# Optimization experiments

Hardware: AMD Instinct MI355X
Metric: run time of the kernel (lower is better)

The kernel has to match this reference:

```python
import jax, jax.numpy as jnp
import numpy as np

EPS = 1e-5

def layer_norm(x, scale, bias):
    mu = jnp.mean(x, axis=-1, keepdims=True)
    var = jnp.var(x, axis=-1, keepdims=True)
    return (x - mu) * jax.lax.rsqrt(var + EPS) * scale + bias

def setup_inputs() -> dict:
    key = jax.random.key(0)
    ks = jax.random.split(key, 12)
    b, l, c_in, c_mid = 1, 512, 128, 128
    act = jax.random.normal(ks[0], (b, l, l, c_in), dtype=jnp.float32)
    mask = jnp.ones((b, l), dtype=jnp.float32)
    sd_in = 1.0 / np.sqrt(c_in)
    sd_mid = 1.0 / np.sqrt(c_mid)
    return {
        "act": act,
        "mask": mask,
        "norm_scale": jnp.ones((c_in,), jnp.float32),
        "norm_bias": jnp.zeros((c_in,), jnp.float32),
        "w_left": jax.random.normal(ks[1], (c_in, c_mid), jnp.float32) * sd_in,
        "b_left": jnp.zeros((c_mid,), jnp.float32),
        "w_right": jax.random.normal(ks[2], (c_in, c_mid), jnp.float32) * sd_in,
        "b_right": jnp.zeros((c_mid,), jnp.float32),
        "w_lgate": jax.random.normal(ks[3], (c_in, c_mid), jnp.float32) * sd_in,
        "b_lgate": jnp.ones((c_mid,), jnp.float32),  # gate init bias=1
        "w_rgate": jax.random.normal(ks[4], (c_in, c_mid), jnp.float32) * sd_in,
        "b_rgate": jnp.ones((c_mid,), jnp.float32),
        "fnorm_scale": jnp.ones((c_mid,), jnp.float32),
        "fnorm_bias": jnp.zeros((c_mid,), jnp.float32),
        "w_out": jax.random.normal(ks[5], (c_mid, c_in), jnp.float32) * sd_mid,
        "b_out": jnp.zeros((c_in,), jnp.float32),
        "w_fgate": jax.random.normal(ks[6], (c_in, c_in), jnp.float32) * sd_in,
        "b_fgate": jnp.ones((c_in,), jnp.float32),
    }

def reference(act, mask, norm_scale, norm_bias, w_left, b_left, w_right, b_right,
              w_lgate, b_lgate, w_rgate, b_rgate, fnorm_scale, fnorm_bias,
              w_out, b_out, w_fgate, b_fgate):
    # pair_mask: (b,l,l,1)
    pair_mask = mask[:, :, None, None] * mask[:, None, :, None]
    x = layer_norm(act, norm_scale, norm_bias)  # (b,l,l,c_in)
    input_act = x
    left = (x @ w_left + b_left) * pair_mask
    right = (x @ w_right + b_right) * pair_mask
    left = left * jax.nn.sigmoid(x @ w_lgate + b_lgate)
    right = right * jax.nn.sigmoid(x @ w_rgate + b_rgate)
    # per_row orientation
    out = jnp.einsum('bikc,bjkc->bijc', left, right)
    out = layer_norm(out, fnorm_scale, fnorm_bias)
    out = out @ w_out + b_out
    out = out * jax.nn.sigmoid(input_act @ w_fgate + b_fgate)
    return out
```

## Files before the change

kernel.cpp:

```cpp
#include <hip/hip_runtime.h>
#include <hip/hip_bf16.h>
#include <stdint.h>

#define LDIM 512
#define CDIM 128
#define NPOS (LDIM*LDIM)

typedef __attribute__((ext_vector_type(8))) short bf16x8;
typedef __attribute__((ext_vector_type(4))) float f32x4;

__device__ __forceinline__ unsigned short f2bf(float f) {
  union { __hip_bfloat16 h; unsigned short u; } cv;
  cv.h = __float2bfloat16(f);
  return cv.u;
}

__device__ __forceinline__ float bf2f(unsigned short u) {
  union { unsigned int i; float f; } cv; cv.i = ((unsigned int)u) << 16; return cv.f;
}

__device__ __forceinline__ float sigm(float x) { return 1.0f / (1.0f + __expf(-x)); }

__device__ __forceinline__ void gl_lds16(const unsigned short* g, unsigned short* l) {
  __builtin_amdgcn_global_load_lds(
      (const __attribute__((address_space(1))) unsigned int*)g,
      (__attribute__((address_space(3))) unsigned int*)l, 16, 0, 0);
}

__global__ __launch_bounds__(256) void k_prep(
    const float* w0, const float* w1, const float* w2,
    const float* w3, const float* w4, const float* w5,
    unsigned short* wtall) {
  __shared__ float tmp[CDIM*CDIM];
  const float* w = (blockIdx.x==0)?w0:(blockIdx.x==1)?w1:(blockIdx.x==2)?w2:
                   (blockIdx.x==3)?w3:(blockIdx.x==4)?w4:w5;
  int t = threadIdx.x;
  #pragma unroll
  for (int m = 0; m < 16; ++m)
    ((float4*)tmp)[m*256 + t] = ((const float4*)w)[m*256 + t];
  __syncthreads();
  unsigned short* out = wtall + (size_t)blockIdx.x * (CDIM*CDIM);
  #pragma unroll
  for (int m = 0; m < 8; ++m) {
    int oc = m*256 + t;
    int n = oc >> 4, sc = oc & 15;
    int s = sc ^ (n & 7);
    union { unsigned short u[8]; uint4 v; } pk;
    #pragma unroll
    for (int e = 0; e < 8; ++e) pk.u[e] = f2bf(tmp[(s*8 + e)*CDIM + n]);
    *(uint4*)(out + (size_t)oc*8) = pk.v;
  }
}

__global__ __launch_bounds__(256,8) void k_ln(
    const float* __restrict__ act,
    const float* __restrict__ nscale, const float* __restrict__ nbias,
    unsigned short* __restrict__ xbf) {
  const int t = threadIdx.x;
  const int pos = blockIdx.x * 64 + (t >> 2), qq = t & 3;
  const int s = pos & 7;

  float4 av[8];
  const float4* ap = (const float4*)(act + (size_t)pos*CDIM);
  #pragma unroll
  for (int cc = 0; cc < 4; ++cc) {
    int ch = cc*4 + qq;
    av[cc*2]     = ap[ch*2];
    av[cc*2 + 1] = ap[ch*2 + 1];
  }

  float sm = 0.f, s2 = 0.f;
  #pragma unroll
  for (int j = 0; j < 8; ++j) {
    float4 v = av[j];
    sm += v.x + v.y + v.z + v.w;
    s2 += v.x*v.x + v.y*v.y + v.z*v.z + v.w*v.w;
  }
  sm += __shfl_xor(sm, 1); s2 += __shfl_xor(s2, 1);
  sm += __shfl_xor(sm, 2); s2 += __shfl_xor(s2, 2);
  float mu = sm * 0.0078125f;
  float rs = rsqrtf(fmaxf(s2 * 0.0078125f - mu*mu, 0.f) + 1e-5f);

  unsigned short* xp = xbf + (size_t)pos * CDIM;
  #pragma unroll
  for (int cc = 0; cc < 4; ++cc) {
    int ch = cc*4 + qq;
    union { unsigned short u[8]; uint4 v; } pk;
    #pragma unroll
    for (int e2 = 0; e2 < 2; ++e2) {
      float4 v = av[cc*2 + e2];
      float4 fs = ((const float4*)nscale)[ch*2 + e2];
      float4 fb = ((const float4*)nbias)[ch*2 + e2];
      int b = e2*4;
      pk.u[b+0] = f2bf((v.x - mu)*rs*fs.x + fb.x);
      pk.u[b+1] = f2bf((v.y - mu)*rs*fs.y + fb.y);
      pk.u[b+2] = f2bf((v.z - mu)*rs*fs.z + fb.z);
      pk.u[b+3] = f2bf((v.w - mu)*rs*fs.w + fb.w);
    }
    int slot = ch ^ s;
    *(uint4*)(xp + slot*8) = pk.v;
  }
}

__global__ __launch_bounds__(512,4) void k_proj(
    const unsigned short* __restrict__ xbf,
    const float* __restrict__ mask,
    const float* __restrict__ b_left, const float* __restrict__ b_lgate,
    const float* __restrict__ b_right, const float* __restrict__ b_rgate,
    const unsigned short* __restrict__ wtall,
    unsigned short* __restrict__ leftT,
    unsigned short* __restrict__ rightT) {
  __shared__ unsigned short WB[2*128*128];
  __shared__ unsigned short xs[64*128];
  const int t = threadIdx.x, wave = t >> 6, lane = t & 63;
  const int fr = lane & 15, kg = lane >> 4;
  const int rg = wave >> 1, cg = wave & 1;
  const int ar = rg*16 + fr;
  const int rbase = rg*16 + kg*4;

  const int side = blockIdx.x >> 9;
  const unsigned short* W = wtall + (size_t)side * 2 * 16384;
  const float* bv = side ? b_right : b_left;
  const float* bg = side ? b_rgate : b_lgate;
  unsigned short* dst = side ? rightT : leftT;

  #pragma unroll
  for (int m = 0; m < 8; ++m) {
    int qb = m*512 + wave*64;
    gl_lds16(W + (size_t)(qb + lane)*8, WB + qb*8);
  }

  const int tile0 = (blockIdx.x & 511) * 8;
  uint4 xr0, xr1;
  {
    const uint4* src = (const uint4*)(xbf + (size_t)tile0*64*CDIM);
    xr0 = src[t*2]; xr1 = src[t*2 + 1];
  }

  for (int tt = 0; tt < 8; ++tt) {
    const int p0 = (tile0 + tt) * 64;
    *(uint4*)(xs + t*16)     = xr0;
    *(uint4*)(xs + t*16 + 8) = xr1;
    __syncthreads();

    if (tt < 7) {
      const uint4* src = (const uint4*)(xbf + (size_t)(p0 + 64)*CDIM);
      xr0 = src[t*2]; xr1 = src[t*2 + 1];
    }

    bf16x8 afr[4];
    #pragma unroll
    for (int ks = 0; ks < 4; ++ks)
      afr[ks] = *(const bf16x8*)(xs + ar*128 + (((ks*4 + kg) ^ (ar & 7)) * 8));

    f32x4 acc[2][4];
    const f32x4 fz = {0.f,0.f,0.f,0.f};
    #pragma unroll
    for (int wi = 0; wi < 2; ++wi) {
      #pragma unroll
      for (int nf = 0; nf < 4; ++nf) {
        acc[wi][nf] = fz;
        int n = cg*64 + nf*16 + fr;
        const unsigned short* Wp = WB + wi*16384 + n*128;
        #pragma unroll
        for (int ks = 0; ks < 4; ++ks) {
          bf16x8 b = *(const bf16x8*)(Wp + (((ks*4 + kg) ^ (n & 7)) * 8));
          acc[wi][nf] = __builtin_amdgcn_mfma_f32_16x16x32_bf16(afr[ks], b, acc[wi][nf], 0,0,0);
        }
      }
    }

    float mi = mask[p0 >> 9];
    float pm[4];
    #pragma unroll
    for (int jj = 0; jj < 4; ++jj)
      pm[jj] = mi * mask[(p0 & 511) + rbase + jj];
    #pragma unroll
    for (int nf = 0; nf < 4; ++nf) {
      int n = cg*64 + nf*16 + fr;
      float bvn = bv[n], bgn = bg[n];
      union { unsigned short u[4]; uint2 v; } pl;
      #pragma unroll
      for (int jj = 0; jj < 4; ++jj)
        pl.u[jj] = f2bf((acc[0][nf][jj] + bvn) * pm[jj] * sigm(acc[1][nf][jj] + bgn));
      *(uint2*)(dst + (size_t)n*NPOS + p0 + rbase) = pl.v;
    }
    if (tt < 7) __syncthreads();
  }
}

__global__ __launch_bounds__(256,2) void k_einsum(
    const unsigned short* __restrict__ leftT,
    const unsigned short* __restrict__ rightT,
    unsigned short* __restrict__ eout) {
  __shared__ unsigned short At[2][128*64];
  __shared__ unsigned short Bt[2][128*64];
  const int t = threadIdx.x, wave = t >> 6, lane = t & 63;
  int fl = (blockIdx.x & 7) * 256 + (blockIdx.x >> 3);
  const int c = fl >> 4;
  const int i0 = ((fl >> 2) & 3) * 128, j0 = (fl & 3) * 128;
  const unsigned short* Lp = leftT + (size_t)c * NPOS;
  const unsigned short* Rp = rightT + (size_t)c * NPOS;
  const int wrow = (wave >> 1) * 64, wcol = (wave & 1) * 64;
  const int kg = lane >> 4, fr = lane & 15;

  f32x4 acc[4][4];
  const f32x4 fz = {0.f,0.f,0.f,0.f};
  #pragma unroll
  for (int a = 0; a < 4; ++a)
    #pragma unroll
    for (int b = 0; b < 4; ++b) acc[a][b] = fz;

  #define STAGE(buf, kt) do {                                              \
    _Pragma("unroll")                                                      \
    for (int m = 0; m < 4; ++m) {                                          \
      int qb = m*256 + wave*64;                                            \
      int qq = qb + lane;                                                  \
      int r = qq >> 3;                                                     \
      int kk = (qq & 7) ^ (r & 7);                                         \
      gl_lds16(Lp + ((size_t)(i0 + r) << 9) + (kt)*64 + kk*8, At[buf] + qb*8); \
      gl_lds16(Rp + ((size_t)(j0 + r) << 9) + (kt)*64 + kk*8, Bt[buf] + qb*8); \
    }                                                                      \
  } while (0)

  STAGE(0, 0);
  __syncthreads();
  int cur = 0;
  for (int kt = 0; kt < 8; ++kt) {
    if (kt < 7) STAGE(cur ^ 1, kt + 1);
    #pragma unroll
    for (int ks = 0; ks < 2; ++ks) {
      bf16x8 af[4], bfr[4];
      #pragma unroll
      for (int mf = 0; mf < 4; ++mf) {
        int r = wrow + mf*16 + fr;
        af[mf] = *(const bf16x8*)(At[cur] + r*64 + (((ks*4 + kg) ^ (r & 7)) * 8));
      }
      #pragma unroll
      for (int nf = 0; nf < 4; ++nf) {
        int r = wcol + nf*16 + fr;
        bfr[nf] = *(const bf16x8*)(Bt[cur] + r*64 + (((ks*4 + kg) ^ (r & 7)) * 8));
      }
      #pragma unroll
      for (int mf = 0; mf < 4; ++mf)
        #pragma unroll
        for (int nf = 0; nf < 4; ++nf)
          acc[mf][nf] = __builtin_amdgcn_mfma_f32_16x16x32_bf16(af[mf], bfr[nf], acc[mf][nf], 0,0,0);
    }
    __syncthreads();
    cur ^= 1;
  }
  #undef STAGE

  unsigned short* bounce = &At[0][0];
  const int rb = kg << 2;
  #pragma unroll
  for (int mf = 0; mf < 4; ++mf) {
    #pragma unroll
    for (int nf = 0; nf < 4; ++nf) {
      #pragma unroll
      for (int jj = 0; jj < 4; ++jj) {
        int ri = wrow + mf*16 + rb + jj;
        int ci = wcol + nf*16 + fr;
        bounce[ri*128 + (((ci >> 3) ^ (ri & 7)) << 3) + (ci & 7)] = f2bf(acc[mf][nf][jj]);
      }
    }
  }
  __syncthreads();
  unsigned short* op = eout + (size_t)c * NPOS;
  #pragma unroll
  for (int rr = 0; rr < 8; ++rr) {
    int flat = rr*256 + t;
    int row = flat >> 4, ch = flat & 15;
    uint4 v = *(const uint4*)(bounce + row*128 + ((ch ^ (row & 7)) << 3));
    *(uint4*)(op + (size_t)(i0 + row)*LDIM + j0 + ch*8) = v;
  }
}

__global__ __launch_bounds__(256,2) void k_stageC(
    const unsigned short* __restrict__ eout,
    const unsigned short* __restrict__ xbf,
    const unsigned short* __restrict__ wtall,
    const float* __restrict__ fns, const float* __restrict__ fnb,
    const float* __restrict__ b_out, const float* __restrict__ b_fg,
    float* __restrict__ outp) {
  __shared__ unsigned short xs[64*128];
  __shared__ unsigned short WB[2][128*128];
  const int t = threadIdx.x, wave = t >> 6, lane = t & 63;
  const int p0 = blockIdx.x * 64;

  #pragma unroll
  for (int m = 0; m < 4; ++m) {
    int qb = m*256 + wave*64;
    gl_lds16(xbf + (size_t)p0*128 + (size_t)(qb + lane)*8, xs + qb*8);
  }
  #pragma unroll
  for (int m = 0; m < 8; ++m) {
    int qb = m*256 + wave*64;
    gl_lds16(wtall + 5*16384 + (size_t)(qb + lane)*8, WB[0] + qb*8);
    gl_lds16(wtall + 4*16384 + (size_t)(qb + lane)*8, WB[1] + qb*8);
  }

  const int pos = t >> 2, qq = t & 3;
  float ev[32];
  const unsigned short* ep = eout + p0 + pos;
  #pragma unroll
  for (int j = 0; j < 32; ++j) ev[j] = bf2f(ep[(size_t)(qq*32 + j) * NPOS]);

  float s = 0.f, s2 = 0.f;
  #pragma unroll
  for (int j = 0; j < 32; ++j) { s += ev[j]; s2 += ev[j]*ev[j]; }
  s += __shfl_xor(s, 1); s2 += __shfl_xor(s2, 1);
  s += __shfl_xor(s, 2); s2 += __shfl_xor(s2, 2);
  float mu = s * 0.0078125f;
  float rs = rsqrtf(fmaxf(s2 * 0.0078125f - mu*mu, 0.f) + 1e-5f);
  unsigned short ybf[32];
  #pragma unroll
  for (int jc = 0; jc < 8; ++jc) {
    float4 fsv = ((const float4*)fns)[qq*8 + jc];
    float4 fbv = ((const float4*)fnb)[qq*8 + jc];
    ybf[jc*4+0] = f2bf((ev[jc*4+0]-mu)*rs*fsv.x + fbv.x);
    ybf[jc*4+1] = f2bf((ev[jc*4+1]-mu)*rs*fsv.y + fbv.y);
    ybf[jc*4+2] = f2bf((ev[jc*4+2]-mu)*rs*fsv.z + fbv.z);
    ybf[jc*4+3] = f2bf((ev[jc*4+3]-mu)*rs*fsv.w + fbv.w);
  }
  __syncthreads();

  const int ar = wave*16 + (lane & 15), kg = lane >> 4, bn = lane & 15;
  bf16x8 afr[4];
  #pragma unroll
  for (int ks = 0; ks < 4; ++ks)
    afr[ks] = *(const bf16x8*)(xs + ar*128 + (((ks*4 + kg) ^ (ar & 7)) * 8));

  f32x4 accG[8], accY[8];
  const f32x4 fz = {0.f,0.f,0.f,0.f};
  #pragma unroll
  for (int nf = 0; nf < 8; ++nf) {
    accG[nf] = fz;
    int n = nf*16 + bn;
    #pragma unroll
    for (int ks = 0; ks < 4; ++ks) {
      bf16x8 b = *(const bf16x8*)(WB[0] + n*128 + (((ks*4 + kg) ^ (n & 7)) * 8));
      accG[nf] = __builtin_amdgcn_mfma_f32_16x16x32_bf16(afr[ks], b, accG[nf], 0,0,0);
    }
  }
  __syncthreads();

  #pragma unroll
  for (int cc = 0; cc < 4; ++cc) {
    int swz = ((qq*4 + cc) ^ (pos & 7));
    union { unsigned short u[8]; uint4 v; } pk;
    #pragma unroll
    for (int e = 0; e < 8; ++e) pk.u[e] = ybf[cc*8 + e];
    *(uint4*)(xs + pos*128 + swz*8) = pk.v;
  }
  __syncthreads();

  bf16x8 yfr[4];
  #pragma unroll
  for (int ks = 0; ks < 4; ++ks)
    yfr[ks] = *(const bf16x8*)(xs + ar*128 + (((ks*4 + kg) ^ (ar & 7)) * 8));
  #pragma unroll
  for (int nf = 0; nf < 8; ++nf) {
    accY[nf] = fz;
    int n = nf*16 + bn;
    #pragma unroll
    for (int ks = 0; ks < 4; ++ks) {
      bf16x8 b = *(const bf16x8*)(WB[1] + n*128 + (((ks*4 + kg) ^ (n & 7)) * 8));
      accY[nf] = __builtin_amdgcn_mfma_f32_16x16x32_bf16(yfr[ks], b, accY[nf], 0,0,0);
    }
  }

  const int rbase = wave*16 + (kg << 2);
  #pragma unroll
  for (int nf = 0; nf < 8; ++nf) {
    int n = nf*16 + bn;
    float bo = b_out[n], bfg = b_fg[n];
    #pragma unroll
    for (int jj = 0; jj < 4; ++jj) {
      float val = (accY[nf][jj] + bo) * sigm(accG[nf][jj] + bfg);
      outp[(size_t)(p0 + rbase + jj)*CDIM + n] = val;
    }
  }
}

extern "C" void kernel_launch(void* const* d_in, const int* in_sizes, int n_in,
                              void* d_out, int out_size, void* d_ws, size_t ws_size,
                              hipStream_t stream) {
  const float* act  = (const float*)d_in[0];
  const float* mask = (const float*)d_in[1];
  const float* nsc  = (const float*)d_in[2];
  const float* nbi  = (const float*)d_in[3];
  const float* w_l  = (const float*)d_in[4];
  const float* b_l  = (const float*)d_in[5];
  const float* w_r  = (const float*)d_in[6];
  const float* b_r  = (const float*)d_in[7];
  const float* w_lg = (const float*)d_in[8];
  const float* b_lg = (const float*)d_in[9];
  const float* w_rg = (const float*)d_in[10];
  const float* b_rg = (const float*)d_in[11];
  const float* fns  = (const float*)d_in[12];
  const float* fnb  = (const float*)d_in[13];
  const float* w_o  = (const float*)d_in[14];
  const float* b_o  = (const float*)d_in[15];
  const float* w_fg = (const float*)d_in[16];
  const float* b_fg = (const float*)d_in[17];
  float* outp = (float*)d_out;

  char* ws = (char*)d_ws;
  unsigned short* xbf    = (unsigned short*)ws;
  unsigned short* leftT  = (unsigned short*)(ws + ((size_t)64 << 20));
  unsigned short* rightT = (unsigned short*)(ws + ((size_t)128 << 20));
  unsigned short* eout   = (unsigned short*)(ws + ((size_t)192 << 20));
  unsigned short* wtall  = (unsigned short*)(ws + ((size_t)320 << 20));

  k_prep<<<6, 256, 0, stream>>>(w_l, w_lg, w_r, w_rg, w_o, w_fg, wtall);
  k_ln<<<NPOS/64, 256, 0, stream>>>(act, nsc, nbi, xbf);
  k_proj<<<1024, 512, 0, stream>>>(xbf, mask, b_l, b_lg, b_r, b_rg, wtall, leftT, rightT);
  k_einsum<<<2048, 256, 0, stream>>>(leftT, rightT, eout);
  k_stageC<<<NPOS/64, 256, 0, stream>>>(eout, xbf, wtall, fns, fnb, b_o, b_fg, outp);
}
```

Baseline: 272.8 us.

## Stage eout tile through LDS with coalesced loads and reuse one weight buffer

In stage C, the channel-major eout tile is now copied into LDS with 16-byte global-to-LDS loads, replacing per-thread strided 2-byte global reads. Layernorm statistics are reduced across waves through a small LDS array. The normalized values are written back into the same LDS tile in swizzled row layout. The two weight matrices now share one LDS buffer, loaded one after the other, which cuts LDS use and may raise occupancy. The cost is extra barriers and a serialized second weight load between the two GEMMs.

```diff
diff --git a/kernel.cpp b/kernel.cpp
--- a/kernel.cpp
+++ b/kernel.cpp
@@ -285,7 +285,9 @@
     const float* __restrict__ b_out, const float* __restrict__ b_fg,
     float* __restrict__ outp) {
   __shared__ unsigned short xs[64*128];
-  __shared__ unsigned short WB[2][128*128];
+  __shared__ unsigned short es[64*128];
+  __shared__ unsigned short WB[128*128];
+  __shared__ float psum[2][4][64];
   const int t = threadIdx.x, wave = t >> 6, lane = t & 63;
   const int p0 = blockIdx.x * 64;
 
@@ -297,34 +299,31 @@
   #pragma unroll
   for (int m = 0; m < 8; ++m) {
     int qb = m*256 + wave*64;
-    gl_lds16(wtall + 5*16384 + (size_t)(qb + lane)*8, WB[0] + qb*8);
-    gl_lds16(wtall + 4*16384 + (size_t)(qb + lane)*8, WB[1] + qb*8);
-  }
-
-  const int pos = t >> 2, qq = t & 3;
+    gl_lds16(wtall + 5*16384 + (size_t)(qb + lane)*8, WB + qb*8);
+  }
+  #pragma unroll
+  for (int m = 0; m < 4; ++m) {
+    int qb = m*256 + wave*64;
+    int q = qb + lane;
+    gl_lds16(eout + (size_t)(q >> 3)*NPOS + p0 + (q & 7)*8, es + qb*8);
+  }
+  __syncthreads();
+
   float ev[32];
-  const unsigned short* ep = eout + p0 + pos;
-  #pragma unroll
-  for (int j = 0; j < 32; ++j) ev[j] = bf2f(ep[(size_t)(qq*32 + j) * NPOS]);
+  #pragma unroll
+  for (int j = 0; j < 32; ++j)
+    ev[j] = bf2f(es[(wave*32 + j)*64 + lane]);
 
   float s = 0.f, s2 = 0.f;
   #pragma unroll
   for (int j = 0; j < 32; ++j) { s += ev[j]; s2 += ev[j]*ev[j]; }
-  s += __shfl_xor(s, 1); s2 += __shfl_xor(s2, 1);
-  s += __shfl_xor(s, 2); s2 += __shfl_xor(s2, 2);
-  float mu = s * 0.0078125f;
-  float rs = rsqrtf(fmaxf(s2 * 0.0078125f - mu*mu, 0.f) + 1e-5f);
-  unsigned short ybf[32];
-  #pragma unroll
-  for (int jc = 0; jc < 8; ++jc) {
-    float4 fsv = ((const float4*)fns)[qq*8 + jc];
-    float4 fbv = ((const float4*)fnb)[qq*8 + jc];
-    ybf[jc*4+0] = f2bf((ev[jc*4+0]-mu)*rs*fsv.x + fbv.x);
-    ybf[jc*4+1] = f2bf((ev[jc*4+1]-mu)*rs*fsv.y + fbv.y);
-    ybf[jc*4+2] = f2bf((ev[jc*4+2]-mu)*rs*fsv.z + fbv.z);
-    ybf[jc*4+3] = f2bf((ev[jc*4+3]-mu)*rs*fsv.w + fbv.w);
-  }
-  __syncthreads();
+  psum[0][wave][lane] = s;
+  psum[1][wave][lane] = s2;
+  __syncthreads();
+  float st  = psum[0][0][lane] + psum[0][1][lane] + psum[0][2][lane] + psum[0][3][lane];
+  float s2t = psum[1][0][lane] + psum[1][1][lane] + psum[1][2][lane] + psum[1][3][lane];
+  float mu = st * 0.0078125f;
+  float rs = rsqrtf(fmaxf(s2t * 0.0078125f - mu*mu, 0.f) + 1e-5f);
 
   const int ar = wave*16 + (lane & 15), kg = lane >> 4, bn = lane & 15;
   bf16x8 afr[4];
@@ -340,33 +339,42 @@
     int n = nf*16 + bn;
     #pragma unroll
     for (int ks = 0; ks < 4; ++ks) {
-      bf16x8 b = *(const bf16x8*)(WB[0] + n*128 + (((ks*4 + kg) ^ (n & 7)) * 8));
+      bf16x8 b = *(const bf16x8*)(WB + n*128 + (((ks*4 + kg) ^ (n & 7)) * 8));
       accG[nf] = __builtin_amdgcn_mfma_f32_16x16x32_bf16(afr[ks], b, accG[nf], 0,0,0);
     }
   }
-  __syncthreads();
-
-  #pragma unroll
-  for (int cc = 0; cc < 4; ++cc) {
-    int swz = ((qq*4 + cc) ^ (pos & 7));
+
+  #pragma unroll
+  for (int k = 0; k < 4; ++k) {
     union { unsigned short u[8]; uint4 v; } pk;
     #pragma unroll
-    for (int e = 0; e < 8; ++e) pk.u[e] = ybf[cc*8 + e];
-    *(uint4*)(xs + pos*128 + swz*8) = pk.v;
+    for (int e = 0; e < 8; ++e) {
+      int c = wave*32 + k*8 + e;
+      pk.u[e] = f2bf((ev[k*8 + e] - mu)*rs*fns[c] + fnb[c]);
+    }
+    int slot = (wave*4 + k) ^ (lane & 7);
+    *(uint4*)(es + lane*128 + slot*8) = pk.v;
+  }
+  __syncthreads();
+
+  #pragma unroll
+  for (int m = 0; m < 8; ++m) {
+    int qb = m*256 + wave*64;
+    gl_lds16(wtall + 4*16384 + (size_t)(qb + lane)*8, WB + qb*8);
   }
   __syncthreads();
 
   bf16x8 yfr[4];
   #pragma unroll
   for (int ks = 0; ks < 4; ++ks)
-    yfr[ks] = *(const bf16x8*)(xs + ar*128 + (((ks*4 + kg) ^ (ar & 7)) * 8));
+    yfr[ks] = *(const bf16x8*)(es + ar*128 + (((ks*4 + kg) ^ (ar & 7)) * 8));
   #pragma unroll
   for (int nf = 0; nf < 8; ++nf) {
     accY[nf] = fz;
     int n = nf*16 + bn;
     #pragma unroll
     for (int ks = 0; ks < 4; ++ks) {
-      bf16x8 b = *(const bf16x8*)(WB[1] + n*128 + (((ks*4 + kg) ^ (n & 7)) * 8));
+      bf16x8 b = *(const bf16x8*)(WB + n*128 + (((ks*4 + kg) ^ (n & 7)) * 8));
       accY[nf] = __builtin_amdgcn_mfma_f32_16x16x32_bf16(yfr[ks], b, accY[nf], 0,0,0);
     }
   }
```

New measurement: 255.2 us. -6.4%, faster.

## Make stageC persistent over 8 tiles with register-prefetched double buffering

Applied to the files above, without the earlier changes.

The output stage now runs 512 blocks of 512 threads, each handling 8 consecutive 64-position tiles. The two 128x128 weight matrices are loaded into LDS once per block instead of once per tile. The next tile's x and einsum-output data are prefetched into registers while the current tile computes, then written into the other LDS buffer. The einsum output is read with coalesced 16-byte loads into LDS, and the layer-norm statistics are reduced across waves through shared memory. This lowers weight reload traffic and hides global latency, at the cost of more LDS per block (about 100KB, which limits occupancy) and extra barriers.

```diff
diff --git a/kernel.cpp b/kernel.cpp
--- a/kernel.cpp
+++ b/kernel.cpp
@@ -277,109 +277,137 @@
   }
 }
 
-__global__ __launch_bounds__(256,2) void k_stageC(
+__global__ __launch_bounds__(512,2) void k_stageC(
     const unsigned short* __restrict__ eout,
     const unsigned short* __restrict__ xbf,
     const unsigned short* __restrict__ wtall,
     const float* __restrict__ fns, const float* __restrict__ fnb,
     const float* __restrict__ b_out, const float* __restrict__ b_fg,
     float* __restrict__ outp) {
-  __shared__ unsigned short xs[64*128];
   __shared__ unsigned short WB[2][128*128];
+  __shared__ unsigned short xs[2][64*128];
+  __shared__ unsigned short es[2][64*128];
+  __shared__ float psum[2][8][64];
   const int t = threadIdx.x, wave = t >> 6, lane = t & 63;
-  const int p0 = blockIdx.x * 64;
+  const int fr = lane & 15, kg = lane >> 4;
+  const int rg = wave >> 1, cg = wave & 1;
+  const int ar = rg*16 + fr;
+  const int rbase = rg*16 + kg*4;
 
   #pragma unroll
   for (int m = 0; m < 4; ++m) {
-    int qb = m*256 + wave*64;
-    gl_lds16(xbf + (size_t)p0*128 + (size_t)(qb + lane)*8, xs + qb*8);
-  }
-  #pragma unroll
-  for (int m = 0; m < 8; ++m) {
-    int qb = m*256 + wave*64;
+    int qb = m*512 + wave*64;
     gl_lds16(wtall + 5*16384 + (size_t)(qb + lane)*8, WB[0] + qb*8);
     gl_lds16(wtall + 4*16384 + (size_t)(qb + lane)*8, WB[1] + qb*8);
   }
 
-  const int pos = t >> 2, qq = t & 3;
-  float ev[32];
-  const unsigned short* ep = eout + p0 + pos;
-  #pragma unroll
-  for (int j = 0; j < 32; ++j) ev[j] = bf2f(ep[(size_t)(qq*32 + j) * NPOS]);
-
-  float s = 0.f, s2 = 0.f;
-  #pragma unroll
-  for (int j = 0; j < 32; ++j) { s += ev[j]; s2 += ev[j]*ev[j]; }
-  s += __shfl_xor(s, 1); s2 += __shfl_xor(s2, 1);
-  s += __shfl_xor(s, 2); s2 += __shfl_xor(s2, 2);
-  float mu = s * 0.0078125f;
-  float rs = rsqrtf(fmaxf(s2 * 0.0078125f - mu*mu, 0.f) + 1e-5f);
-  unsigned short ybf[32];
-  #pragma unroll
-  for (int jc = 0; jc < 8; ++jc) {
-    float4 fsv = ((const float4*)fns)[qq*8 + jc];
-    float4 fbv = ((const float4*)fnb)[qq*8 + jc];
-    ybf[jc*4+0] = f2bf((ev[jc*4+0]-mu)*rs*fsv.x + fbv.x);
-    ybf[jc*4+1] = f2bf((ev[jc*4+1]-mu)*rs*fsv.y + fbv.y);
-    ybf[jc*4+2] = f2bf((ev[jc*4+2]-mu)*rs*fsv.z + fbv.z);
-    ybf[jc*4+3] = f2bf((ev[jc*4+3]-mu)*rs*fsv.w + fbv.w);
-  }
-  __syncthreads();
-
-  const int ar = wave*16 + (lane & 15), kg = lane >> 4, bn = lane & 15;
-  bf16x8 afr[4];
-  #pragma unroll
-  for (int ks = 0; ks < 4; ++ks)
-    afr[ks] = *(const bf16x8*)(xs + ar*128 + (((ks*4 + kg) ^ (ar & 7)) * 8));
-
-  f32x4 accG[8], accY[8];
+  const int tile0 = blockIdx.x * 8;
+  uint4 xr0, xr1, er0, er1;
+  {
+    const uint4* xsrc = (const uint4*)(xbf + (size_t)tile0*64*CDIM);
+    xr0 = xsrc[t]; xr1 = xsrc[512 + t];
+    const unsigned short* eb = eout + (size_t)tile0*64;
+    er0 = *(const uint4*)(eb + (size_t)(t >> 3)*NPOS + (t & 7)*8);
+    er1 = *(const uint4*)(eb + (size_t)(64 + (t >> 3))*NPOS + (t & 7)*8);
+  }
+  *(uint4*)(xs[0] + t*8) = xr0; *(uint4*)(xs[0] + 4096 + t*8) = xr1;
+  *(uint4*)(es[0] + t*8) = er0; *(uint4*)(es[0] + 4096 + t*8) = er1;
+
+  int cur = 0;
   const f32x4 fz = {0.f,0.f,0.f,0.f};
-  #pragma unroll
-  for (int nf = 0; nf < 8; ++nf) {
-    accG[nf] = fz;
-    int n = nf*16 + bn;
-    #pragma unroll
-    for (int ks = 0; ks < 4; ++ks) {
-      bf16x8 b = *(const bf16x8*)(WB[0] + n*128 + (((ks*4 + kg) ^ (n & 7)) * 8));
-      accG[nf] = __builtin_amdgcn_mfma_f32_16x16x32_bf16(afr[ks], b, accG[nf], 0,0,0);
-    }
-  }
-  __syncthreads();
-
-  #pragma unroll
-  for (int cc = 0; cc < 4; ++cc) {
-    int swz = ((qq*4 + cc) ^ (pos & 7));
-    union { unsigned short u[8]; uint4 v; } pk;
-    #pragma unroll
-    for (int e = 0; e < 8; ++e) pk.u[e] = ybf[cc*8 + e];
-    *(uint4*)(xs + pos*128 + swz*8) = pk.v;
-  }
-  __syncthreads();
-
-  bf16x8 yfr[4];
-  #pragma unroll
-  for (int ks = 0; ks < 4; ++ks)
-    yfr[ks] = *(const bf16x8*)(xs + ar*128 + (((ks*4 + kg) ^ (ar & 7)) * 8));
-  #pragma unroll
-  for (int nf = 0; nf < 8; ++nf) {
-    accY[nf] = fz;
-    int n = nf*16 + bn;
-    #pragma unroll
-    for (int ks = 0; ks < 4; ++ks) {
-      bf16x8 b = *(const bf16x8*)(WB[1] + n*128 + (((ks*4 + kg) ^ (n & 7)) * 8));
-      accY[nf] = __builtin_amdgcn_mfma_f32_16x16x32_bf16(yfr[ks], b, accY[nf], 0,0,0);
-    }
-  }
-
-  const int rbase = wave*16 + (kg << 2);
-  #pragma unroll
-  for (int nf = 0; nf < 8; ++nf) {
-    int n = nf*16 + bn;
-    float bo = b_out[n], bfg = b_fg[n];
-    #pragma unroll
-    for (int jj = 0; jj < 4; ++jj) {
-      float val = (accY[nf][jj] + bo) * sigm(accG[nf][jj] + bfg);
-      outp[(size_t)(p0 + rbase + jj)*CDIM + n] = val;
+  for (int tt = 0; tt < 8; ++tt) {
+    const int p0 = (tile0 + tt) * 64;
+    __syncthreads();
+
+    if (tt < 7) {
+      const uint4* xsrc = (const uint4*)(xbf + (size_t)(p0 + 64)*CDIM);
+      xr0 = xsrc[t]; xr1 = xsrc[512 + t];
+      const unsigned short* eb = eout + (size_t)(p0 + 64);
+      er0 = *(const uint4*)(eb + (size_t)(t >> 3)*NPOS + (t & 7)*8);
+      er1 = *(const uint4*)(eb + (size_t)(64 + (t >> 3))*NPOS + (t & 7)*8);
+    }
+
+    float ev[16];
+    #pragma unroll
+    for (int j = 0; j < 16; ++j)
+      ev[j] = bf2f(es[cur][(wave*16 + j)*64 + lane]);
+    float s = 0.f, s2 = 0.f;
+    #pragma unroll
+    for (int j = 0; j < 16; ++j) { s += ev[j]; s2 += ev[j]*ev[j]; }
+    psum[0][wave][lane] = s; psum[1][wave][lane] = s2;
+    __syncthreads();
+    float st = 0.f, s2t = 0.f;
+    #pragma unroll
+    for (int w = 0; w < 8; ++w) { st += psum[0][w][lane]; s2t += psum[1][w][lane]; }
+    float mu = st * 0.0078125f;
+    float rs = rsqrtf(fmaxf(s2t * 0.0078125f - mu*mu, 0.f) + 1e-5f);
+
+    bf16x8 afr[4];
+    #pragma unroll
+    for (int ks = 0; ks < 4; ++ks)
+      afr[ks] = *(const bf16x8*)(xs[cur] + ar*128 + (((ks*4 + kg) ^ (ar & 7)) * 8));
+
+    f32x4 accG[4], accY[4];
+    #pragma unroll
+    for (int nf = 0; nf < 4; ++nf) {
+      accG[nf] = fz;
+      int n = cg*64 + nf*16 + fr;
+      #pragma unroll
+      for (int ks = 0; ks < 4; ++ks) {
+        bf16x8 b = *(const bf16x8*)(WB[0] + n*128 + (((ks*4 + kg) ^ (n & 7)) * 8));
+        accG[nf] = __builtin_amdgcn_mfma_f32_16x16x32_bf16(afr[ks], b, accG[nf], 0,0,0);
+      }
+    }
+
+    #pragma unroll
+    for (int k = 0; k < 2; ++k) {
+      union { unsigned short u[8]; uint4 v; } pk;
+      #pragma unroll
+      for (int e4 = 0; e4 < 2; ++e4) {
+        float4 fsv = ((const float4*)fns)[wave*4 + k*2 + e4];
+        float4 fbv = ((const float4*)fnb)[wave*4 + k*2 + e4];
+        int j = k*8 + e4*4;
+        pk.u[e4*4+0] = f2bf((ev[j+0]-mu)*rs*fsv.x + fbv.x);
+        pk.u[e4*4+1] = f2bf((ev[j+1]-mu)*rs*fsv.y + fbv.y);
+        pk.u[e4*4+2] = f2bf((ev[j+2]-mu)*rs*fsv.z + fbv.z);
+        pk.u[e4*4+3] = f2bf((ev[j+3]-mu)*rs*fsv.w + fbv.w);
+      }
+      int ch = wave*2 + k;
+      int slot = ch ^ (lane & 7);
+      *(uint4*)(es[cur] + lane*128 + slot*8) = pk.v;
+    }
+    __syncthreads();
+
+    bf16x8 yfr[4];
+    #pragma unroll
+    for (int ks = 0; ks < 4; ++ks)
+      yfr[ks] = *(const bf16x8*)(es[cur] + ar*128 + (((ks*4 + kg) ^ (ar & 7)) * 8));
+    #pragma unroll
+    for (int nf = 0; nf < 4; ++nf) {
+      accY[nf] = fz;
+      int n = cg*64 + nf*16 + fr;
+      #pragma unroll
+      for (int ks = 0; ks < 4; ++ks) {
+        bf16x8 b = *(const bf16x8*)(WB[1] + n*128 + (((ks*4 + kg) ^ (n & 7)) * 8));
+        accY[nf] = __builtin_amdgcn_mfma_f32_16x16x32_bf16(yfr[ks], b, accY[nf], 0,0,0);
+      }
+    }
+
+    #pragma unroll
+    for (int nf = 0; nf < 4; ++nf) {
+      int n = cg*64 + nf*16 + fr;
+      float bo = b_out[n], bfg = b_fg[n];
+      #pragma unroll
+      for (int jj = 0; jj < 4; ++jj) {
+        float val = (accY[nf][jj] + bo) * sigm(accG[nf][jj] + bfg);
+        outp[(size_t)(p0 + rbase + jj)*CDIM + n] = val;
+      }
+    }
+
+    if (tt < 7) {
+      *(uint4*)(xs[cur^1] + t*8) = xr0; *(uint4*)(xs[cur^1] + 4096 + t*8) = xr1;
+      *(uint4*)(es[cur^1] + t*8) = er0; *(uint4*)(es[cur^1] + 4096 + t*8) = er1;
+      cur ^= 1;
     }
   }
 }
@@ -418,5 +446,5 @@
   k_ln<<<NPOS/64, 256, 0, stream>>>(act, nsc, nbi, xbf);
   k_proj<<<1024, 512, 0, stream>>>(xbf, mask, b_l, b_lg, b_r, b_rg, wtall, leftT, rightT);
   k_einsum<<<2048, 256, 0, stream>>>(leftT, rightT, eout);
-  k_stageC<<<NPOS/64, 256, 0, stream>>>(eout, xbf, wtall, fns, fnb, b_o, b_fg, outp);
-}
+  k_stageC<<<512, 512, 0, stream>>>(eout, xbf, wtall, fns, fnb, b_o, b_fg, outp);
+}
```

After: 243.7 us, median of 3. -10.7%, faster.
